# Kernel tuning notes

Hardware: AMD Instinct MI355X
Metric: run time of the kernel (lower is better)

The kernel has to match this reference:

```python
import jax, jax.numpy as jnp
import numpy as np

B, T, D, H, E = 4, 2048, 1024, 4096, 8


def setup_inputs() -> dict:
    key = jax.random.key(0)
    ks = jax.random.split(key, 7)
    x = jax.random.normal(ks[0], (B, T, D), dtype=jnp.float32)
    # Gate: Linear(D, E)
    Wg = jax.random.normal(ks[1], (D, E), dtype=jnp.float32) / np.sqrt(D)
    bg = jax.random.normal(ks[2], (E,), dtype=jnp.float32) * 0.01
    # Experts: E x [Linear(D,H), ReLU, Linear(H,D)] (dropout inactive at eval)
    W1 = jax.random.normal(ks[3], (E, D, H), dtype=jnp.float32) / np.sqrt(D)
    b1 = jax.random.normal(ks[4], (E, H), dtype=jnp.float32) * 0.01
    W2 = jax.random.normal(ks[5], (E, H, D), dtype=jnp.float32) / np.sqrt(H)
    b2 = jax.random.normal(ks[6], (E, D), dtype=jnp.float32) * 0.01
    return {"x": x, "Wg": Wg, "bg": bg, "W1": W1, "b1": b1, "W2": W2, "b2": b2}


def reference(x, Wg, bg, W1, b1, W2, b2):
    # Gate + hard top-1 routing
    gate_scores = x @ Wg + bg                      # [B,T,E]
    top1 = jnp.argmax(gate_scores, axis=-1)        # [B,T]
    onehot = jax.nn.one_hot(top1, Wg.shape[-1], dtype=x.dtype)  # [B,T,E]
    # Dense: every expert MLP over all tokens (matches original's masked
    # formulation: x*mask == x on selected tokens, output re-masked).
    h = jax.nn.relu(jnp.einsum('btd,edh->beth', x, W1) + b1[None, :, None, :])
    y = jnp.einsum('beth,ehd->betd', h, W2) + b2[None, :, None, :]
    # Masked combine: keep only the token's chosen expert output
    out = jnp.einsum('betd,bte->btd', y, onehot)
    return out
```

## Files before the change

### kernel.cpp

```cpp
#include <hip/hip_runtime.h>
#include <hip/hip_bf16.h>
#include <stdint.h>

#define NTOK 8192
#define DDIM 1024
#define HDIM 4096
#define NEXP 8
#define MAXWL1 48
#define MAXWL2 72

typedef __attribute__((ext_vector_type(4))) float f32x4;
typedef __attribute__((ext_vector_type(8))) short s16x8;
typedef __attribute__((ext_vector_type(8))) unsigned short u16x8;

__device__ __forceinline__ unsigned short f2bf(float f) {
  union { float f; unsigned int u; } v; v.f = f;
  unsigned int u = v.u;
  u += 0x7FFFu + ((u >> 16) & 1u);
  return (unsigned short)(u >> 16);
}

typedef __attribute__((address_space(3))) unsigned char lds_u8;
typedef const __attribute__((address_space(1))) unsigned char glb_u8;

__device__ __forceinline__ void load_lds16(const void* g, void* l) {
  __builtin_amdgcn_global_load_lds((glb_u8*)g, (lds_u8*)l, 16, 0, 0);
}

__global__ __launch_bounds__(256) void gate_kernel(
    const float* __restrict__ x, const float* __restrict__ Wg,
    const float* __restrict__ bg, int* __restrict__ counts,
    int* __restrict__ lists) {
  const int lane = threadIdx.x & 63;
  const int tok = blockIdx.x * 4 + (threadIdx.x >> 6);
  const float* xr = x + (size_t)tok * DDIM;
  double acc[NEXP];
#pragma unroll
  for (int e = 0; e < NEXP; ++e) acc[e] = 0.0;
#pragma unroll 4
  for (int it = 0; it < DDIM / 64; ++it) {
    const int d = it * 64 + lane;
    const float xv = xr[d];
    const f32x4 w0 = *(const f32x4*)(Wg + (size_t)d * NEXP);
    const f32x4 w1 = *(const f32x4*)(Wg + (size_t)d * NEXP + 4);
#pragma unroll
    for (int j = 0; j < 4; ++j) {
      acc[j]     += (double)xv * (double)w0[j];
      acc[4 + j] += (double)xv * (double)w1[j];
    }
  }
#pragma unroll
  for (int e = 0; e < NEXP; ++e) {
    double v = acc[e];
#pragma unroll
    for (int off = 32; off > 0; off >>= 1) v += __shfl_xor(v, off, 64);
    acc[e] = v;
  }
  if (lane == 0) {
    int best = 0;
    double bv = acc[0] + (double)bg[0];
#pragma unroll
    for (int e = 1; e < NEXP; ++e) {
      const double v = acc[e] + (double)bg[e];
      if (v > bv) { bv = v; best = e; }
    }
    const int pos = atomicAdd(&counts[best], 1);
    lists[best * NTOK + pos] = tok;
  }
}

__global__ void offs_kernel(const int* __restrict__ counts, int* __restrict__ offs,
                            int* __restrict__ wl1, int* __restrict__ wl2) {
  int s = 0;
#pragma unroll
  for (int e = 0; e < NEXP; ++e) { offs[e] = s; s += counts[e]; }
  offs[NEXP] = s;
  int n1 = 0, n2 = 0;
  for (int e = 0; e < NEXP; ++e) {
    const int nb1 = (counts[e] + 255) >> 8;
    for (int b = 0; b < nb1; ++b) wl1[n1++] = (e << 20) | b;
    const int nb2 = (counts[e] + 127) >> 7;
    for (int b = 0; b < nb2; ++b) wl2[n2++] = (e << 20) | b;
  }
  offs[NEXP + 1] = n1;
  offs[NEXP + 2] = n2;
}

__global__ __launch_bounds__(256) void gather_conv_kernel(
    const float* __restrict__ x, const int* __restrict__ offs,
    const int* __restrict__ lists, int* __restrict__ stok,
    unsigned short* __restrict__ xbs) {
  const int p = blockIdx.x * 4 + (threadIdx.x >> 6);
  const int lane = threadIdx.x & 63;
  int e = 0;
#pragma unroll
  for (int k = 1; k < NEXP; ++k) e += (p >= offs[k]) ? 1 : 0;
  const int tok = lists[e * NTOK + (p - offs[e])];
  if (lane == 0) stok[p] = tok;
  const float* src = x + (size_t)tok * DDIM + lane * 16;
  unsigned short* dst = xbs + (size_t)p * DDIM + lane * 16;
#pragma unroll
  for (int q = 0; q < 2; ++q) {
    const f32x4 a = *(const f32x4*)(src + q * 8);
    const f32x4 b = *(const f32x4*)(src + q * 8 + 4);
    u16x8 o;
#pragma unroll
    for (int j = 0; j < 4; ++j) { o[j] = f2bf(a[j]); o[4 + j] = f2bf(b[j]); }
    *(u16x8*)(dst + q * 8) = o;
  }
}

__global__ __launch_bounds__(256) void transpose_conv_kernel(
    const float* __restrict__ in, unsigned short* __restrict__ out,
    int R, int C) {
  __shared__ unsigned short T[64][66];
  const int e = blockIdx.z;
  const float* ine = in + (size_t)e * R * C;
  unsigned short* oute = out + (size_t)e * C * R;
  const int c0 = blockIdx.x * 64, r0 = blockIdx.y * 64;
  const int t = threadIdx.x;
  const int tr = t >> 4, tc4 = (t & 15) * 4;
#pragma unroll
  for (int p = 0; p < 4; ++p) {
    const int r = tr + p * 16;
    const f32x4 v = *(const f32x4*)(ine + (size_t)(r0 + r) * C + c0 + tc4);
#pragma unroll
    for (int j = 0; j < 4; ++j) T[r][tc4 + j] = f2bf(v[j]);
  }
  __syncthreads();
  const int cc = t >> 3, rr8 = (t & 7) * 8;
#pragma unroll
  for (int p = 0; p < 2; ++p) {
    const int c = cc + p * 32;
    u16x8 o;
#pragma unroll
    for (int j = 0; j < 8; ++j) o[j] = T[rr8 + j][c];
    *(u16x8*)(oute + (size_t)(c0 + c) * R + r0 + rr8) = o;
  }
}

template <int BM, int BN, int WN, int K, int N, int MAXWLT, bool FUSE1>
__global__ __launch_bounds__(512, 2) void ffn_kernel(
    const unsigned short* __restrict__ A, const unsigned short* __restrict__ Bt,
    const float* __restrict__ bias, const int* __restrict__ counts,
    const int* __restrict__ offs, const int* __restrict__ wl,
    const int* __restrict__ stok, unsigned short* __restrict__ outb,
    float* __restrict__ outf, int nwl_idx) {
  constexpr int WM = 8 / WN;
  constexpr int MF = BM / (WM * 16);
  constexpr int NF = BN / (WN * 16);
  constexpr int ISS_A = BM / 128;
  constexpr int ISS_B = BN / 128;
  constexpr int NT = K / 32;
  constexpr int NCB = N / BN;
  constexpr int NWG = NCB * MAXWLT;
  static_assert((NWG & 7) == 0 && (NT & 1) == 0 && NT >= 4, "");

  const int d = blockIdx.x;
  const int logical = (d & 7) * (NWG / 8) + (d >> 3);
  const int col0 = (logical / MAXWLT) * BN;
  const int wli = logical % MAXWLT;
  if (wli >= offs[nwl_idx]) return;
  const int wle = wl[wli];
  const int e = wle >> 20;
  const int bx = wle & 0xFFFFF;
  const int cnt = counts[e];
  const int row0 = offs[e] + bx * BM;

  __shared__ __align__(16) unsigned short As0[BM * 32], Bs0[BN * 32];
  __shared__ __align__(16) unsigned short As1[BM * 32], Bs1[BN * 32];

  const int tid = threadIdx.x;
  const int lane = tid & 63;
  const int w = tid >> 6;
  const int wm = w / WN;
  const int wn = w % WN;
  const int fr = lane & 15;
  const int fj = lane >> 4;

  const int kslot = (tid & 3) * 8;
  const int rb = tid >> 2;
  const unsigned short* srcA[ISS_A];
#pragma unroll
  for (int i = 0; i < ISS_A; ++i) {
    int gr = row0 + i * 128 + rb;
    if (gr > NTOK - 1) gr = NTOK - 1;
    srcA[i] = A + (size_t)gr * K + kslot;
  }
  const unsigned short* Bte = Bt + (size_t)e * N * K;
  const unsigned short* srcB[ISS_B];
#pragma unroll
  for (int i = 0; i < ISS_B; ++i)
    srcB[i] = Bte + (size_t)(col0 + i * 128 + rb) * K + kslot;

  f32x4 acc[MF][NF];
#pragma unroll
  for (int m = 0; m < MF; ++m)
#pragma unroll
    for (int n = 0; n < NF; ++n) acc[m][n] = f32x4{0.f, 0.f, 0.f, 0.f};

  auto stage = [&](unsigned short* dA, unsigned short* dB, int kel) {
#pragma unroll
    for (int i = 0; i < ISS_A; ++i)
      load_lds16(srcA[i] + kel, dA + i * 128 * 32 + tid * 8);
#pragma unroll
    for (int i = 0; i < ISS_B; ++i)
      load_lds16(srcB[i] + kel, dB + i * 128 * 32 + tid * 8);
  };

  auto body = [&](const unsigned short* pA, const unsigned short* pB,
                  unsigned short* nA, unsigned short* nB, int knext,
                  bool do_stage) {
    asm volatile("s_waitcnt vmcnt(0)" ::: "memory");
    __builtin_amdgcn_s_barrier();
    asm volatile("" ::: "memory");
    if (do_stage) stage(nA, nB, knext);
    s16x8 af[MF], bf[NF];
#pragma unroll
    for (int m = 0; m < MF; ++m)
      af[m] = *(const s16x8*)(pA + (wm * MF * 16 + m * 16 + fr) * 32 + fj * 8);
#pragma unroll
    for (int n = 0; n < NF; ++n)
      bf[n] = *(const s16x8*)(pB + (wn * NF * 16 + n * 16 + fr) * 32 + fj * 8);
    __builtin_amdgcn_s_setprio(1);
#pragma unroll
    for (int m = 0; m < MF; ++m)
#pragma unroll
      for (int n = 0; n < NF; ++n)
        acc[m][n] = __builtin_amdgcn_mfma_f32_16x16x32_bf16(af[m], bf[n],
                                                            acc[m][n], 0, 0, 0);
    __builtin_amdgcn_s_setprio(0);
  };

  stage(As0, Bs0, 0);
#pragma unroll 1
  for (int t = 0; t < NT - 2; t += 2) {
    body(As0, Bs0, As1, Bs1, (t + 1) * 32, true);
    body(As1, Bs1, As0, Bs0, (t + 2) * 32, true);
  }
  body(As0, Bs0, As1, Bs1, (NT - 1) * 32, true);
  body(As1, Bs1, nullptr, nullptr, 0, false);

#pragma unroll
  for (int n = 0; n < NF; ++n) {
    const int col = col0 + wn * NF * 16 + n * 16 + fr;
    const float bv = bias[e * N + col];
#pragma unroll
    for (int m = 0; m < MF; ++m) {
#pragma unroll
      for (int j = 0; j < 4; ++j) {
        const int rl = wm * MF * 16 + m * 16 + fj * 4 + j;
        if (bx * BM + rl < cnt) {
          if constexpr (FUSE1) {
            outb[(size_t)(row0 + rl) * N + col] = f2bf(fmaxf(acc[m][n][j] + bv, 0.f));
          } else {
            outf[(size_t)stok[row0 + rl] * N + col] = acc[m][n][j] + bv;
          }
        }
      }
    }
  }
}

extern "C" void kernel_launch(void* const* d_in, const int* in_sizes, int n_in,
                              void* d_out, int out_size, void* d_ws, size_t ws_size,
                              hipStream_t stream) {
  (void)in_sizes; (void)n_in; (void)out_size;
  const float* x  = (const float*)d_in[0];
  const float* Wg = (const float*)d_in[1];
  const float* bg = (const float*)d_in[2];
  const float* W1 = (const float*)d_in[3];
  const float* b1 = (const float*)d_in[4];
  const float* W2 = (const float*)d_in[5];
  const float* b2 = (const float*)d_in[6];
  float* out = (float*)d_out;

  char* ws = (char*)d_ws;
  const size_t OFF_CNT = 0;
  const size_t OFF_OFF = 128;
  const size_t OFF_WL1 = 256;
  const size_t OFF_WL2 = 256 + MAXWL1 * 4;
  const size_t OFF_LST = 1024;
  const size_t OFF_STK = OFF_LST + (size_t)NEXP * NTOK * 4;
  const size_t OFF_XBS = OFF_STK + (size_t)NTOK * 4;
  const size_t OFF_HS  = OFF_XBS + (size_t)NTOK * DDIM * 2;
  const size_t OFF_WT  = OFF_HS + (size_t)NTOK * HDIM * 2;
  const size_t NEED    = OFF_WT + (size_t)NEXP * DDIM * HDIM * 2;
  if (ws_size < NEED) return;

  int* counts = (int*)(ws + OFF_CNT);
  int* offs   = (int*)(ws + OFF_OFF);
  int* wl1    = (int*)(ws + OFF_WL1);
  int* wl2    = (int*)(ws + OFF_WL2);
  int* lists  = (int*)(ws + OFF_LST);
  int* stok   = (int*)(ws + OFF_STK);
  unsigned short* xbs = (unsigned short*)(ws + OFF_XBS);
  unsigned short* Hs  = (unsigned short*)(ws + OFF_HS);
  unsigned short* Wt  = (unsigned short*)(ws + OFF_WT);

  hipMemsetAsync(counts, 0, 128, stream);
  gate_kernel<<<NTOK / 4, 256, 0, stream>>>(x, Wg, bg, counts, lists);
  offs_kernel<<<1, 1, 0, stream>>>(counts, offs, wl1, wl2);
  gather_conv_kernel<<<NTOK / 4, 256, 0, stream>>>(x, offs, lists, stok, xbs);

  transpose_conv_kernel<<<dim3(HDIM / 64, DDIM / 64, NEXP), 256, 0, stream>>>(
      W1, Wt, DDIM, HDIM);
  ffn_kernel<256, 256, 4, DDIM, HDIM, MAXWL1, true>
      <<<dim3((HDIM / 256) * MAXWL1), 512, 0, stream>>>(
          xbs, Wt, b1, counts, offs, wl1, stok, Hs, nullptr, NEXP + 1);
  transpose_conv_kernel<<<dim3(DDIM / 64, HDIM / 64, NEXP), 256, 0, stream>>>(
      W2, Wt, HDIM, DDIM);
  ffn_kernel<128, 256, 4, HDIM, DDIM, MAXWL2, false>
      <<<dim3((DDIM / 256) * MAXWL2), 512, 0, stream>>>(
          Hs, Wt, b2, counts, offs, wl2, stok, nullptr, out, NEXP + 2);
}
```

Baseline: 542.4 us.

## Swizzle LDS layout, reorder fragment loads, retile FFN1 and column-fast FFN2 scheduling

Adds an XOR swizzle to the K-slot placement of A and B tiles in LDS, with the matching swizzled fragment read, to cut LDS bank conflicts. Fragment reads from LDS now happen before the next async stage is issued. FFN1 changes from a 256x256 to a 256x128 tile with a 4x2 wave layout, and FFN2 gains a column-fast block order for better A-tile reuse across column blocks. Launch bounds now request 4 blocks per CU, which tightens the register budget and risks spills.

```diff
diff --git a/kernel.cpp b/kernel.cpp
--- a/kernel.cpp
+++ b/kernel.cpp
@@ -139,14 +139,14 @@
   }
 }
 
-template <int BM, int BN, int WN, int K, int N, int MAXWLT, bool FUSE1>
-__global__ __launch_bounds__(512, 2) void ffn_kernel(
+template <int BM, int BN, int WM, int WN, int K, int N, int MAXWLT,
+          bool COLFAST, bool FUSE1>
+__global__ __launch_bounds__(512, 4) void ffn_kernel(
     const unsigned short* __restrict__ A, const unsigned short* __restrict__ Bt,
     const float* __restrict__ bias, const int* __restrict__ counts,
     const int* __restrict__ offs, const int* __restrict__ wl,
     const int* __restrict__ stok, unsigned short* __restrict__ outb,
     float* __restrict__ outf, int nwl_idx) {
-  constexpr int WM = 8 / WN;
   constexpr int MF = BM / (WM * 16);
   constexpr int NF = BN / (WN * 16);
   constexpr int ISS_A = BM / 128;
@@ -155,12 +155,15 @@
   constexpr int NCB = N / BN;
   constexpr int NWG = NCB * MAXWLT;
   static_assert((NWG & 7) == 0 && (NT & 1) == 0 && NT >= 4, "");
+  static_assert(WM * WN == 8, "8 waves");
 
   const int d = blockIdx.x;
   const int logical = (d & 7) * (NWG / 8) + (d >> 3);
-  const int col0 = (logical / MAXWLT) * BN;
-  const int wli = logical % MAXWLT;
+  int cb, wli;
+  if constexpr (COLFAST) { cb = logical % NCB; wli = logical / NCB; }
+  else                   { cb = logical / MAXWLT; wli = logical % MAXWLT; }
   if (wli >= offs[nwl_idx]) return;
+  const int col0 = cb * BN;
   const int wle = wl[wli];
   const int e = wle >> 20;
   const int bx = wle & 0xFFFFF;
@@ -178,20 +181,22 @@
   const int fr = lane & 15;
   const int fj = lane >> 4;
 
-  const int kslot = (tid & 3) * 8;
+  const int swsrc = ((tid & 3) ^ ((tid >> 3) & 3)) * 8;
   const int rb = tid >> 2;
   const unsigned short* srcA[ISS_A];
 #pragma unroll
   for (int i = 0; i < ISS_A; ++i) {
     int gr = row0 + i * 128 + rb;
     if (gr > NTOK - 1) gr = NTOK - 1;
-    srcA[i] = A + (size_t)gr * K + kslot;
+    srcA[i] = A + (size_t)gr * K + swsrc;
   }
   const unsigned short* Bte = Bt + (size_t)e * N * K;
   const unsigned short* srcB[ISS_B];
 #pragma unroll
   for (int i = 0; i < ISS_B; ++i)
-    srcB[i] = Bte + (size_t)(col0 + i * 128 + rb) * K + kslot;
+    srcB[i] = Bte + (size_t)(col0 + i * 128 + rb) * K + swsrc;
+
+  const int js = (fj ^ ((fr >> 1) & 3)) * 8;
 
   f32x4 acc[MF][NF];
 #pragma unroll
@@ -202,26 +207,26 @@
   auto stage = [&](unsigned short* dA, unsigned short* dB, int kel) {
 #pragma unroll
     for (int i = 0; i < ISS_A; ++i)
-      load_lds16(srcA[i] + kel, dA + i * 128 * 32 + tid * 8);
+      load_lds16(srcA[i] + kel, dA + i * 4096 + tid * 8);
 #pragma unroll
     for (int i = 0; i < ISS_B; ++i)
-      load_lds16(srcB[i] + kel, dB + i * 128 * 32 + tid * 8);
+      load_lds16(srcB[i] + kel, dB + i * 4096 + tid * 8);
   };
 
-  auto body = [&](const unsigned short* pA, const unsigned short* pB,
-                  unsigned short* nA, unsigned short* nB, int knext,
-                  bool do_stage) {
+  auto phase = [&](const unsigned short* pA, const unsigned short* pB,
+                   unsigned short* nA, unsigned short* nB, int knext,
+                   bool do_stage) {
     asm volatile("s_waitcnt vmcnt(0)" ::: "memory");
     __builtin_amdgcn_s_barrier();
     asm volatile("" ::: "memory");
+    s16x8 af[MF], bf[NF];
+#pragma unroll
+    for (int m = 0; m < MF; ++m)
+      af[m] = *(const s16x8*)(pA + (wm * MF * 16 + m * 16 + fr) * 32 + js);
+#pragma unroll
+    for (int n = 0; n < NF; ++n)
+      bf[n] = *(const s16x8*)(pB + (wn * NF * 16 + n * 16 + fr) * 32 + js);
     if (do_stage) stage(nA, nB, knext);
-    s16x8 af[MF], bf[NF];
-#pragma unroll
-    for (int m = 0; m < MF; ++m)
-      af[m] = *(const s16x8*)(pA + (wm * MF * 16 + m * 16 + fr) * 32 + fj * 8);
-#pragma unroll
-    for (int n = 0; n < NF; ++n)
-      bf[n] = *(const s16x8*)(pB + (wn * NF * 16 + n * 16 + fr) * 32 + fj * 8);
     __builtin_amdgcn_s_setprio(1);
 #pragma unroll
     for (int m = 0; m < MF; ++m)
@@ -235,11 +240,11 @@
   stage(As0, Bs0, 0);
 #pragma unroll 1
   for (int t = 0; t < NT - 2; t += 2) {
-    body(As0, Bs0, As1, Bs1, (t + 1) * 32, true);
-    body(As1, Bs1, As0, Bs0, (t + 2) * 32, true);
-  }
-  body(As0, Bs0, As1, Bs1, (NT - 1) * 32, true);
-  body(As1, Bs1, nullptr, nullptr, 0, false);
+    phase(As0, Bs0, As1, Bs1, (t + 1) * 32, true);
+    phase(As1, Bs1, As0, Bs0, (t + 2) * 32, true);
+  }
+  phase(As0, Bs0, As1, Bs1, (NT - 1) * 32, true);
+  phase(As1, Bs1, nullptr, nullptr, 0, false);
 
 #pragma unroll
   for (int n = 0; n < NF; ++n) {
@@ -305,12 +310,12 @@
 
   transpose_conv_kernel<<<dim3(HDIM / 64, DDIM / 64, NEXP), 256, 0, stream>>>(
       W1, Wt, DDIM, HDIM);
-  ffn_kernel<256, 256, 4, DDIM, HDIM, MAXWL1, true>
-      <<<dim3((HDIM / 256) * MAXWL1), 512, 0, stream>>>(
+  ffn_kernel<256, 128, 4, 2, DDIM, HDIM, MAXWL1, false, true>
+      <<<dim3((HDIM / 128) * MAXWL1), 512, 0, stream>>>(
           xbs, Wt, b1, counts, offs, wl1, stok, Hs, nullptr, NEXP + 1);
   transpose_conv_kernel<<<dim3(DDIM / 64, HDIM / 64, NEXP), 256, 0, stream>>>(
       W2, Wt, HDIM, DDIM);
-  ffn_kernel<128, 256, 4, HDIM, DDIM, MAXWL2, false>
+  ffn_kernel<128, 256, 2, 4, HDIM, DDIM, MAXWL2, true, false>
       <<<dim3((DDIM / 256) * MAXWL2), 512, 0, stream>>>(
           Hs, Wt, b2, counts, offs, wl2, stok, nullptr, out, NEXP + 2);
 }
```

After: 453.0 us. 1.2x faster.
